# Kernel optimization log

Hardware: AMD Instinct MI355X
Metric: run time of the kernel (lower is better)

## Reference

```python
import jax, jax.numpy as jnp
import numpy as np

K = 3  # number of propagation hops in SGConv


def setup_inputs() -> dict:
    key = jax.random.key(0)
    k1, k2, k3, k4 = jax.random.split(key, 4)
    N, E, F_in, F_out = 100000, 1600000, 32, 64
    x = jax.random.normal(k1, (N, F_in), dtype=jnp.float32)
    edge_index = jax.random.randint(k2, (2, E), 0, N, dtype=jnp.int64)
    # Linear(in_channels, hidden_channels) params, torch layout: W [out, in], b [out]
    lim = 1.0 / np.sqrt(F_in)
    W = jax.random.uniform(k3, (F_out, F_in), minval=-lim, maxval=lim, dtype=jnp.float32)
    b = jax.random.uniform(k4, (F_out,), minval=-lim, maxval=lim, dtype=jnp.float32)
    return {"x": x, "edge_index": edge_index, "W": W, "b": b}


def reference(x, edge_index, W, b):
    N = x.shape[0]
    # gcn_norm: add self-loops with weight 1, symmetric normalization
    loop = jnp.arange(N, dtype=edge_index.dtype)
    src = jnp.concatenate([edge_index[0], loop])  # [E+N] message sources (x_j)
    dst = jnp.concatenate([edge_index[1], loop])  # [E+N] aggregation targets
    ones = jnp.ones(src.shape[0], dtype=x.dtype)
    deg = jax.ops.segment_sum(ones, dst, num_segments=N)  # in-degree incl. self-loop
    dinv = jnp.where(deg > 0, jax.lax.rsqrt(deg), 0.0)
    norm = dinv[src] * dinv[dst]  # [E+N]
    # K hops of normalized sparse propagation: x <- \hat{A} x
    h = x
    for _ in range(K):
        h = jax.ops.segment_sum(norm[:, None] * h[src], dst, num_segments=N)
    # final linear transform
    return h @ W.T + b
```

## Files before the change

kernel.cpp:

```cpp
#include <hip/hip_runtime.h>


#define F_IN 32
#define F_OUT 64
#define SB_SHIFT 13
#define NSB_MAX 16
#define SUB_SHIFT 8
#define SUB (1 << SUB_SHIFT)
#define SPS 32
#define EPB1 2048
#define EPB2 4096
#define SCAP 147456
#define SUBCAP 6144
#define BPS (SCAP / EPB2)

typedef float f4 __attribute__((ext_vector_type(4)));
typedef float f8 __attribute__((ext_vector_type(8)));
typedef _Float16 h4 __attribute__((ext_vector_type(4)));
typedef _Float16 h8 __attribute__((ext_vector_type(8)));
typedef int i2 __attribute__((ext_vector_type(2)));

__global__ __launch_bounds__(256) void k_bin1(const int* __restrict__ ei,
                                              int* __restrict__ scur,
                                              unsigned* __restrict__ b1, int E) {
    __shared__ unsigned stage[EPB1];
    __shared__ unsigned char bidl[EPB1];
    __shared__ int h4w[4][NSB_MAX];
    __shared__ int f4w[4][NSB_MAX];
    __shared__ int lscanx[NSB_MAX], lbase[NSB_MAX];
    unsigned rec[EPB1 / 256];
    int      bk[EPB1 / 256];
    int tid = threadIdx.x;
    int wv = tid >> 6;
    int base = blockIdx.x * EPB1;
    int cnt = E - base; if (cnt > EPB1) cnt = EPB1;

    if (tid < 64) { h4w[tid >> 4][tid & 15] = 0; }
    __syncthreads();
#pragma unroll
    for (int k = 0; k < EPB1 / 256; ++k) {
        int i = base + k * 256 + tid;
        bk[k] = -1;
        if (i < E) {
            unsigned s = (unsigned)ei[i];
            unsigned d = (unsigned)ei[E + i];
            int b = d >> SB_SHIFT;
            rec[k] = (s << SB_SHIFT) | (d & ((1u << SB_SHIFT) - 1));
            bk[k] = b;
            atomicAdd(&h4w[wv][b], 1);
        }
    }
    __syncthreads();
    if (tid < 16) {
        int t0 = h4w[0][tid], t1 = h4w[1][tid], t2 = h4w[2][tid], t3 = h4w[3][tid];
        int tot = t0 + t1 + t2 + t3;
        int inc = tot;
#pragma unroll
        for (int off = 1; off < 16; off <<= 1) {
            int t = __shfl_up(inc, off);
            if (tid >= off) inc += t;
        }
        int excl = inc - tot;
        lscanx[tid] = excl;
        lbase[tid] = tot ? atomicAdd(&scur[tid], tot) : 0;
        f4w[0][tid] = excl;
        f4w[1][tid] = excl + t0;
        f4w[2][tid] = excl + t0 + t1;
        f4w[3][tid] = excl + t0 + t1 + t2;
    }
    __syncthreads();
#pragma unroll
    for (int k = 0; k < EPB1 / 256; ++k) {
        if (bk[k] >= 0) {
            int loc = atomicAdd(&f4w[wv][bk[k]], 1);
            stage[loc] = rec[k];
            bidl[loc] = (unsigned char)bk[k];
        }
    }
    __syncthreads();
    for (int k = 0; k < EPB1 / 256; ++k) {
        int idx = k * 256 + tid;
        if (idx < cnt) {
            int b = bidl[idx];
            b1[(size_t)b * SCAP + lbase[b] + (idx - lscanx[b])] = stage[idx];
        }
    }
}

__global__ __launch_bounds__(256) void k_bin2(const unsigned* __restrict__ b1,
                                              const int* __restrict__ scur,
                                              int* __restrict__ subcur,
                                              unsigned* __restrict__ b2) {
    int sb = blockIdx.x / BPS;
    int base = (blockIdx.x % BPS) * EPB2;
    int count = scur[sb];
    if (base >= count) return;
    int cnt = count - base; if (cnt > EPB2) cnt = EPB2;
    const unsigned* src = b1 + (size_t)sb * SCAP + base;

    __shared__ unsigned stage[EPB2];
    __shared__ unsigned char bidl[EPB2];
    __shared__ int h4w[4][SPS];
    __shared__ int f4w[4][SPS];
    __shared__ int lscanx[SPS], lbase[SPS];
    unsigned rec[EPB2 / 256];
    int tid = threadIdx.x;
    int wv = tid >> 6;
    if (tid < 128) h4w[tid >> 5][tid & 31] = 0;
    __syncthreads();
#pragma unroll
    for (int k = 0; k < EPB2 / 256; ++k) {
        int i = k * 256 + tid;
        rec[k] = 0xFFFFFFFFu;
        if (i < cnt) {
            unsigned r = src[i];
            rec[k] = r;
            atomicAdd(&h4w[wv][(r >> SUB_SHIFT) & (SPS - 1)], 1);
        }
    }
    __syncthreads();
    if (tid < 32) {
        int t0 = h4w[0][tid], t1 = h4w[1][tid], t2 = h4w[2][tid], t3 = h4w[3][tid];
        int tot = t0 + t1 + t2 + t3;
        int inc = tot;
#pragma unroll
        for (int off = 1; off < 32; off <<= 1) {
            int t = __shfl_up(inc, off);
            if (tid >= off) inc += t;
        }
        int excl = inc - tot;
        lscanx[tid] = excl;
        lbase[tid] = tot ? atomicAdd(&subcur[sb * SPS + tid], tot) : 0;
        f4w[0][tid] = excl;
        f4w[1][tid] = excl + t0;
        f4w[2][tid] = excl + t0 + t1;
        f4w[3][tid] = excl + t0 + t1 + t2;
    }
    __syncthreads();
#pragma unroll
    for (int k = 0; k < EPB2 / 256; ++k) {
        if (rec[k] != 0xFFFFFFFFu) {
            int b = (rec[k] >> SUB_SHIFT) & (SPS - 1);
            int loc = atomicAdd(&f4w[wv][b], 1);
            stage[loc] = rec[k];
            bidl[loc] = (unsigned char)b;
        }
    }
    __syncthreads();
    for (int k = 0; k < EPB2 / 256; ++k) {
        int idx = k * 256 + tid;
        if (idx < cnt) {
            unsigned r = stage[idx];
            int b = bidl[idx];
            unsigned packed = ((r >> SB_SHIFT) << SUB_SHIFT) | (r & (SUB - 1));
            b2[(size_t)(sb * SPS + b) * SUBCAP + lbase[b] + (idx - lscanx[b])] = packed;
        }
    }
}

__global__ __launch_bounds__(256) void k_fill3(const unsigned* __restrict__ b2,
                                               const int* __restrict__ subcur,
                                               const f4* __restrict__ x,
                                               float* __restrict__ dinv,
                                               i2* __restrict__ rp2,
                                               int* __restrict__ col,
                                               h8* __restrict__ g0, int N) {
    __shared__ unsigned stage[SUBCAP];
    __shared__ int h[SUB];
    __shared__ float dl[SUB];
    __shared__ int wsum[4];
    int tid = threadIdx.x;
    int g = blockIdx.x;
    int count = subcur[g];
    int sbase = g * SUBCAP;
    int n0 = g << SUB_SHIFT;

    h[tid] = 0;
    for (int e = tid; e < count; e += 256) stage[e] = b2[(size_t)sbase + e];
    __syncthreads();
    for (int e = tid; e < count; e += 256) atomicAdd(&h[stage[e] & (SUB - 1)], 1);
    __syncthreads();

    int deg = h[tid];
    int lane = tid & 63, wid = tid >> 6;
    int inc = deg;
#pragma unroll
    for (int off = 1; off < 64; off <<= 1) {
        int t = __shfl_up(inc, off);
        if (lane >= off) inc += t;
    }
    if (lane == 63) wsum[wid] = inc;
    __syncthreads();
    if (wid == 0) {
        int v = (lane < 4) ? wsum[lane] : 0;
#pragma unroll
        for (int off = 1; off < 4; off <<= 1) {
            int t = __shfl_up(v, off);
            if (lane >= off) v += t;
        }
        if (lane < 4) wsum[lane] = v;
    }
    __syncthreads();
    int incl = inc + (wid ? wsum[wid - 1] : 0);
    int excl = incl - deg;

    int node = n0 + tid;
    float di = rsqrtf(1.0f + (float)deg);
    dl[tid] = di;
    if (node < N) {
        dinv[node] = di;
        rp2[node] = (i2){sbase + excl, sbase + incl};
    }
    h[tid] = excl;
    __syncthreads();

    for (int e = tid; e < count; e += 256) {
        unsigned r = stage[e];
        int slot = sbase + atomicAdd(&h[r & (SUB - 1)], 1);
        col[slot] = (int)(r >> SUB_SHIFT);
    }

    for (int idx = tid; idx < SUB * 4; idx += 256) {
        int nl = idx >> 2;
        int q = idx & 3;
        int node2 = n0 + nl;
        if (node2 < N) {
            int gi = node2 * 8 + q * 2;
            f4 vlo = dl[nl] * x[gi];
            f4 vhi = dl[nl] * x[gi + 1];
            f8 v = __builtin_shufflevector(vlo, vhi, 0, 1, 2, 3, 4, 5, 6, 7);
            g0[(size_t)node2 * 4 + q] = __builtin_convertvector(v, h8);
        }
    }
}

__global__ __launch_bounds__(256) void k_hop_gather(const i2* __restrict__ rp2,
                                                    const int* __restrict__ col,
                                                    const float* __restrict__ dinv,
                                                    const h8* __restrict__ gin,
                                                    h8* __restrict__ gout, int N) {
    int t = blockIdx.x * blockDim.x + threadIdx.x;
    int n = t >> 2;
    if (n >= N) return;
    int q = t & 3;
    i2 r2 = rp2[n];
    int e0 = r2.x, e1 = r2.y;
    f8 a0 = __builtin_convertvector(gin[(size_t)n * 4 + q], f8);
    f8 a1 = {0.f, 0.f, 0.f, 0.f, 0.f, 0.f, 0.f, 0.f};
    int e = e0;
    for (; e + 3 < e1; e += 4) {
        int s0 = col[e], s1 = col[e + 1], s2 = col[e + 2], s3 = col[e + 3];
        h8 h0 = gin[(size_t)s0 * 4 + q];
        h8 h1 = gin[(size_t)s1 * 4 + q];
        h8 h2 = gin[(size_t)s2 * 4 + q];
        h8 h3 = gin[(size_t)s3 * 4 + q];
        a0 += __builtin_convertvector(h0, f8);
        a1 += __builtin_convertvector(h1, f8);
        a0 += __builtin_convertvector(h2, f8);
        a1 += __builtin_convertvector(h3, f8);
    }
    for (; e < e1; ++e) a0 += __builtin_convertvector(gin[(size_t)col[e] * 4 + q], f8);
    float di = dinv[n];
    float sc = di * di;
    f8 r = sc * (a0 + a1);
    gout[(size_t)n * 4 + q] = __builtin_convertvector(r, h8);
}

__global__ __launch_bounds__(256) void k_hop3_linear(const i2* __restrict__ rp2,
                                                     const int* __restrict__ col,
                                                     const float* __restrict__ dinv,
                                                     const h8* __restrict__ gin,
                                                     const float* __restrict__ W,
                                                     const float* __restrict__ bias,
                                                     float* __restrict__ out, int N) {
    __shared__ float Wl[F_OUT][F_IN + 1];
    __shared__ float hl[64][F_IN + 1];
    int tid = threadIdx.x;
    for (int idx = tid; idx < F_OUT * F_IN; idx += 256)
        Wl[idx >> 5][idx & 31] = W[idx];

    int nl = tid >> 2;
    int q = tid & 3;
    int nbase = blockIdx.x * 64;
    int n = nbase + nl;
    if (n < N) {
        i2 r2 = rp2[n];
        int e0 = r2.x, e1 = r2.y;
        f8 a0 = __builtin_convertvector(gin[(size_t)n * 4 + q], f8);
        f8 a1 = {0.f, 0.f, 0.f, 0.f, 0.f, 0.f, 0.f, 0.f};
        int e = e0;
        for (; e + 3 < e1; e += 4) {
            int s0 = col[e], s1 = col[e + 1], s2 = col[e + 2], s3 = col[e + 3];
            h8 h0 = gin[(size_t)s0 * 4 + q];
            h8 h1 = gin[(size_t)s1 * 4 + q];
            h8 h2 = gin[(size_t)s2 * 4 + q];
            h8 h3 = gin[(size_t)s3 * 4 + q];
            a0 += __builtin_convertvector(h0, f8);
            a1 += __builtin_convertvector(h1, f8);
            a0 += __builtin_convertvector(h2, f8);
            a1 += __builtin_convertvector(h3, f8);
        }
        for (; e < e1; ++e) a0 += __builtin_convertvector(gin[(size_t)col[e] * 4 + q], f8);
        float di = dinv[n];
        f8 r = di * (a0 + a1);
#pragma unroll
        for (int i = 0; i < 8; ++i) hl[nl][q * 8 + i] = r[i];
    }
    __syncthreads();
    int o = tid & 63;
    float wreg[F_IN];
#pragma unroll
    for (int f = 0; f < F_IN; ++f) wreg[f] = Wl[o][f];
    float bv = bias[o];
    int nchunk = tid >> 6;
#pragma unroll
    for (int p = 0; p < 16; ++p) {
        int nloc = p * 4 + nchunk;
        int nn = nbase + nloc;
        if (nn < N) {
            float acc = bv;
#pragma unroll
            for (int f = 0; f < F_IN; ++f) acc += hl[nloc][f] * wreg[f];
            out[(size_t)nn * F_OUT + o] = acc;
        }
    }
}

extern "C" void kernel_launch(void* const* d_in, const int* in_sizes, int n_in,
                              void* d_out, int out_size, void* d_ws, size_t ws_size,
                              hipStream_t stream) {
    const float* x  = (const float*)d_in[0];
    const int*   ei = (const int*)d_in[1];
    const float* W  = (const float*)d_in[2];
    const float* b  = (const float*)d_in[3];
    float* out = (float*)d_out;

    const int N = in_sizes[0] / F_IN;
    const int E = in_sizes[1] / 2;
    const int NSB  = (N + (1 << SB_SHIFT) - 1) >> SB_SHIFT;
    const int NSUB = (N + SUB - 1) >> SUB_SHIFT;

    int* scur   = (int*)d_ws;
    int* subcur = scur + NSB_MAX;
    i2*  rp2    = (i2*)(subcur + NSB_MAX * SPS);
    float* dinv = (float*)(rp2 + N);
    unsigned* b1 = (unsigned*)(((uintptr_t)(dinv + N) + 255) & ~(uintptr_t)255);
    unsigned* b2 = b1 + (size_t)NSB_MAX * SCAP;
    int* col     = (int*)(b2 + (size_t)NSB_MAX * SPS * SUBCAP);
    _Float16* hA = (_Float16*)(((uintptr_t)(col + (size_t)NSB_MAX * SPS * SUBCAP) + 255)
                               & ~(uintptr_t)255);
    _Float16* hB  = hA + (size_t)N * F_IN;
    _Float16* hB2 = hB + (size_t)N * F_IN;

    const int B = 256;
    dim3 blk(B);

    hipMemsetAsync(scur, 0, (NSB_MAX + NSB_MAX * SPS) * sizeof(int), stream);

    k_bin1<<<dim3((E + EPB1 - 1) / EPB1), blk, 0, stream>>>(ei, scur, b1, E);
    k_bin2<<<dim3(NSB * BPS), blk, 0, stream>>>(b1, scur, subcur, b2);

    k_fill3<<<dim3(NSUB), blk, 0, stream>>>(b2, subcur, (const f4*)x,
                                            dinv, rp2, col, (h8*)hA, N);

    dim3 gHop(((size_t)N * 4 + B - 1) / B);
    k_hop_gather<<<gHop, blk, 0, stream>>>(rp2, col, dinv, (const h8*)hA, (h8*)hB, N);
    k_hop_gather<<<gHop, blk, 0, stream>>>(rp2, col, dinv, (const h8*)hB, (h8*)hB2, N);

    k_hop3_linear<<<dim3((N + 63) / 64), blk, 0, stream>>>(rp2, col, dinv,
                                                           (const h8*)hB2, W, b, out, N);
}
```

Measured before the change: 200.3 us.

## Split feature halves into separate arrays and pack per-node CSR records

Features are split into two 16-feature half arrays, each 3.2 MB in fp16. Each hop kernel now processes one half at a time, with block IDs interleaved so that concurrently running blocks touch the same half, which is meant to make gather reads hit in cache. Row pointers and dinv are packed into one int4 record per node, and each row is padded to a multiple of 4 so column indices can be read as int4 loads. The third hop is no longer fused with the linear layer, so a separate k_linear kernel and one extra launch plus a write and read of the intermediate are added.

Result: slower. 225.8 us (+12.7%).

```diff
diff --git a/kernel.cpp b/kernel.cpp
--- a/kernel.cpp
+++ b/kernel.cpp
@@ -16,7 +16,6 @@
 
 typedef float f4 __attribute__((ext_vector_type(4)));
 typedef float f8 __attribute__((ext_vector_type(8)));
-typedef _Float16 h4 __attribute__((ext_vector_type(4)));
 typedef _Float16 h8 __attribute__((ext_vector_type(8)));
 typedef int i2 __attribute__((ext_vector_type(2)));
 
@@ -161,10 +160,10 @@
 __global__ __launch_bounds__(256) void k_fill3(const unsigned* __restrict__ b2,
                                                const int* __restrict__ subcur,
                                                const f4* __restrict__ x,
-                                               float* __restrict__ dinv,
-                                               i2* __restrict__ rp2,
+                                               int4* __restrict__ nrec,
                                                int* __restrict__ col,
-                                               h8* __restrict__ g0, int N) {
+                                               h8* __restrict__ g_lo,
+                                               h8* __restrict__ g_hi, int N) {
     __shared__ unsigned stage[SUBCAP];
     __shared__ int h[SUB];
     __shared__ float dl[SUB];
@@ -182,8 +181,9 @@
     __syncthreads();
 
     int deg = h[tid];
+    int pdeg = (deg + 3) & ~3;
     int lane = tid & 63, wid = tid >> 6;
-    int inc = deg;
+    int inc = pdeg;
 #pragma unroll
     for (int off = 1; off < 64; off <<= 1) {
         int t = __shfl_up(inc, off);
@@ -202,16 +202,16 @@
     }
     __syncthreads();
     int incl = inc + (wid ? wsum[wid - 1] : 0);
-    int excl = incl - deg;
+    int exclp = incl - pdeg;
 
     int node = n0 + tid;
     float di = rsqrtf(1.0f + (float)deg);
     dl[tid] = di;
     if (node < N) {
-        dinv[node] = di;
-        rp2[node] = (i2){sbase + excl, sbase + incl};
-    }
-    h[tid] = excl;
+        int e0a = sbase + exclp;
+        nrec[node] = make_int4(e0a, e0a + deg, __float_as_int(di), 0);
+    }
+    h[tid] = exclp;
     __syncthreads();
 
     for (int e = tid; e < count; e += 256) {
@@ -229,82 +229,75 @@
             f4 vlo = dl[nl] * x[gi];
             f4 vhi = dl[nl] * x[gi + 1];
             f8 v = __builtin_shufflevector(vlo, vhi, 0, 1, 2, 3, 4, 5, 6, 7);
-            g0[(size_t)node2 * 4 + q] = __builtin_convertvector(v, h8);
-        }
-    }
-}
-
-__global__ __launch_bounds__(256) void k_hop_gather(const i2* __restrict__ rp2,
-                                                    const int* __restrict__ col,
-                                                    const float* __restrict__ dinv,
-                                                    const h8* __restrict__ gin,
-                                                    h8* __restrict__ gout, int N) {
-    int t = blockIdx.x * blockDim.x + threadIdx.x;
-    int n = t >> 2;
+            h8 hv = __builtin_convertvector(v, h8);
+            if (q < 2) g_lo[(size_t)node2 * 2 + q] = hv;
+            else       g_hi[(size_t)node2 * 2 + (q - 2)] = hv;
+        }
+    }
+}
+
+__global__ __launch_bounds__(256) void k_hop_half(const int4* __restrict__ nrec,
+                                                  const int* __restrict__ col,
+                                                  const h8* __restrict__ gin_lo,
+                                                  const h8* __restrict__ gin_hi,
+                                                  h8* __restrict__ gout_lo,
+                                                  h8* __restrict__ gout_hi,
+                                                  int N, int hblocks, int isfinal) {
+    int bid = blockIdx.x;
+    int grp = bid & 7;
+    int lblk = (bid >> 3) * 4 + (grp & 3);
+    if (lblk >= hblocks) return;
+    const h8* __restrict__ gin  = (grp < 4) ? gin_lo  : gin_hi;
+    h8*       __restrict__ gout = (grp < 4) ? gout_lo : gout_hi;
+    int t = lblk * 256 + threadIdx.x;
+    int n = t >> 1;
     if (n >= N) return;
-    int q = t & 3;
-    i2 r2 = rp2[n];
-    int e0 = r2.x, e1 = r2.y;
-    f8 a0 = __builtin_convertvector(gin[(size_t)n * 4 + q], f8);
+    int q = t & 1;
+    int4 r = nrec[n];
+    int e0 = r.x, e1 = r.y;
+    float di = __int_as_float(r.z);
+    f8 a0 = __builtin_convertvector(gin[(size_t)n * 2 + q], f8);
     f8 a1 = {0.f, 0.f, 0.f, 0.f, 0.f, 0.f, 0.f, 0.f};
     int e = e0;
     for (; e + 3 < e1; e += 4) {
-        int s0 = col[e], s1 = col[e + 1], s2 = col[e + 2], s3 = col[e + 3];
-        h8 h0 = gin[(size_t)s0 * 4 + q];
-        h8 h1 = gin[(size_t)s1 * 4 + q];
-        h8 h2 = gin[(size_t)s2 * 4 + q];
-        h8 h3 = gin[(size_t)s3 * 4 + q];
+        int4 c4 = *(const int4*)(col + e);
+        h8 h0 = gin[(size_t)c4.x * 2 + q];
+        h8 h1 = gin[(size_t)c4.y * 2 + q];
+        h8 h2 = gin[(size_t)c4.z * 2 + q];
+        h8 h3 = gin[(size_t)c4.w * 2 + q];
         a0 += __builtin_convertvector(h0, f8);
         a1 += __builtin_convertvector(h1, f8);
         a0 += __builtin_convertvector(h2, f8);
         a1 += __builtin_convertvector(h3, f8);
     }
-    for (; e < e1; ++e) a0 += __builtin_convertvector(gin[(size_t)col[e] * 4 + q], f8);
-    float di = dinv[n];
-    float sc = di * di;
-    f8 r = sc * (a0 + a1);
-    gout[(size_t)n * 4 + q] = __builtin_convertvector(r, h8);
-}
-
-__global__ __launch_bounds__(256) void k_hop3_linear(const i2* __restrict__ rp2,
-                                                     const int* __restrict__ col,
-                                                     const float* __restrict__ dinv,
-                                                     const h8* __restrict__ gin,
-                                                     const float* __restrict__ W,
-                                                     const float* __restrict__ bias,
-                                                     float* __restrict__ out, int N) {
+    for (; e < e1; ++e) a0 += __builtin_convertvector(gin[(size_t)col[e] * 2 + q], f8);
+    float sc = isfinal ? di : di * di;
+    f8 rr = sc * (a0 + a1);
+    gout[(size_t)n * 2 + q] = __builtin_convertvector(rr, h8);
+}
+
+__global__ __launch_bounds__(256) void k_linear(const h8* __restrict__ lo,
+                                                const h8* __restrict__ hi,
+                                                const float* __restrict__ W,
+                                                const float* __restrict__ bias,
+                                                float* __restrict__ out, int N) {
     __shared__ float Wl[F_OUT][F_IN + 1];
     __shared__ float hl[64][F_IN + 1];
     int tid = threadIdx.x;
     for (int idx = tid; idx < F_OUT * F_IN; idx += 256)
         Wl[idx >> 5][idx & 31] = W[idx];
 
-    int nl = tid >> 2;
-    int q = tid & 3;
     int nbase = blockIdx.x * 64;
-    int n = nbase + nl;
-    if (n < N) {
-        i2 r2 = rp2[n];
-        int e0 = r2.x, e1 = r2.y;
-        f8 a0 = __builtin_convertvector(gin[(size_t)n * 4 + q], f8);
-        f8 a1 = {0.f, 0.f, 0.f, 0.f, 0.f, 0.f, 0.f, 0.f};
-        int e = e0;
-        for (; e + 3 < e1; e += 4) {
-            int s0 = col[e], s1 = col[e + 1], s2 = col[e + 2], s3 = col[e + 3];
-            h8 h0 = gin[(size_t)s0 * 4 + q];
-            h8 h1 = gin[(size_t)s1 * 4 + q];
-            h8 h2 = gin[(size_t)s2 * 4 + q];
-            h8 h3 = gin[(size_t)s3 * 4 + q];
-            a0 += __builtin_convertvector(h0, f8);
-            a1 += __builtin_convertvector(h1, f8);
-            a0 += __builtin_convertvector(h2, f8);
-            a1 += __builtin_convertvector(h3, f8);
-        }
-        for (; e < e1; ++e) a0 += __builtin_convertvector(gin[(size_t)col[e] * 4 + q], f8);
-        float di = dinv[n];
-        f8 r = di * (a0 + a1);
-#pragma unroll
-        for (int i = 0; i < 8; ++i) hl[nl][q * 8 + i] = r[i];
+    {
+        int nl = tid >> 2;
+        int c = tid & 3;
+        int n = nbase + nl;
+        if (n < N) {
+            h8 v = (c < 2) ? lo[(size_t)n * 2 + c] : hi[(size_t)n * 2 + (c - 2)];
+            f8 f = __builtin_convertvector(v, f8);
+#pragma unroll
+            for (int i = 0; i < 8; ++i) hl[nl][c * 8 + i] = f[i];
+        }
     }
     __syncthreads();
     int o = tid & 63;
@@ -342,15 +335,17 @@
 
     int* scur   = (int*)d_ws;
     int* subcur = scur + NSB_MAX;
-    i2*  rp2    = (i2*)(subcur + NSB_MAX * SPS);
-    float* dinv = (float*)(rp2 + N);
-    unsigned* b1 = (unsigned*)(((uintptr_t)(dinv + N) + 255) & ~(uintptr_t)255);
+    int4* nrec  = (int4*)(((uintptr_t)(subcur + NSB_MAX * SPS) + 255) & ~(uintptr_t)255);
+    unsigned* b1 = (unsigned*)(((uintptr_t)(nrec + N) + 255) & ~(uintptr_t)255);
     unsigned* b2 = b1 + (size_t)NSB_MAX * SCAP;
     int* col     = (int*)(b2 + (size_t)NSB_MAX * SPS * SUBCAP);
-    _Float16* hA = (_Float16*)(((uintptr_t)(col + (size_t)NSB_MAX * SPS * SUBCAP) + 255)
-                               & ~(uintptr_t)255);
-    _Float16* hB  = hA + (size_t)N * F_IN;
-    _Float16* hB2 = hB + (size_t)N * F_IN;
+    _Float16* hbase = (_Float16*)(((uintptr_t)(col + (size_t)NSB_MAX * SPS * SUBCAP) + 255)
+                                  & ~(uintptr_t)255);
+    const size_t HALF = (size_t)N * (F_IN / 2);
+    _Float16* hAlo = hbase;
+    _Float16* hAhi = hAlo + HALF;
+    _Float16* hBlo = hAhi + HALF;
+    _Float16* hBhi = hBlo + HALF;
 
     const int B = 256;
     dim3 blk(B);
@@ -361,12 +356,17 @@
     k_bin2<<<dim3(NSB * BPS), blk, 0, stream>>>(b1, scur, subcur, b2);
 
     k_fill3<<<dim3(NSUB), blk, 0, stream>>>(b2, subcur, (const f4*)x,
-                                            dinv, rp2, col, (h8*)hA, N);
-
-    dim3 gHop(((size_t)N * 4 + B - 1) / B);
-    k_hop_gather<<<gHop, blk, 0, stream>>>(rp2, col, dinv, (const h8*)hA, (h8*)hB, N);
-    k_hop_gather<<<gHop, blk, 0, stream>>>(rp2, col, dinv, (const h8*)hB, (h8*)hB2, N);
-
-    k_hop3_linear<<<dim3((N + 63) / 64), blk, 0, stream>>>(rp2, col, dinv,
-                                                           (const h8*)hB2, W, b, out, N);
-}
+                                            nrec, col, (h8*)hAlo, (h8*)hAhi, N);
+
+    const int HB = (N * 2 + B - 1) / B;
+    dim3 gHop(8 * ((HB + 3) / 4));
+    k_hop_half<<<gHop, blk, 0, stream>>>(nrec, col, (const h8*)hAlo, (const h8*)hAhi,
+                                         (h8*)hBlo, (h8*)hBhi, N, HB, 0);
+    k_hop_half<<<gHop, blk, 0, stream>>>(nrec, col, (const h8*)hBlo, (const h8*)hBhi,
+                                         (h8*)hAlo, (h8*)hAhi, N, HB, 0);
+    k_hop_half<<<gHop, blk, 0, stream>>>(nrec, col, (const h8*)hAlo, (const h8*)hAhi,
+                                         (h8*)hBlo, (h8*)hBhi, N, HB, 1);
+
+    k_linear<<<dim3((N + 63) / 64), blk, 0, stream>>>((const h8*)hBlo, (const h8*)hBhi,
+                                                      W, b, out, N);
+}
```

## Pack node records, pad CSR rows for vector col loads, add nontemporal hints

Applied to the files above, without the earlier changes.

Merges the row-pointer pair and dinv into a single 16-byte per-node record, so one load replaces two. Each node's edge segment is padded to a multiple of four, which lets column indices be fetched as aligned int4 loads with a software-prefetched next group. Nontemporal loads and stores are applied to streaming data (x, col, records, outputs), and the hop buffers are ping-ponged to drop one feature buffer. This cuts load instructions and cache pollution in the gather kernels, at the cost of padding slack in each subgroup's col capacity.

New measurement: 206.7 us. +3.2%, slower.

```diff
diff --git a/kernel.cpp b/kernel.cpp
--- a/kernel.cpp
+++ b/kernel.cpp
@@ -16,9 +16,8 @@
 
 typedef float f4 __attribute__((ext_vector_type(4)));
 typedef float f8 __attribute__((ext_vector_type(8)));
-typedef _Float16 h4 __attribute__((ext_vector_type(4)));
 typedef _Float16 h8 __attribute__((ext_vector_type(8)));
-typedef int i2 __attribute__((ext_vector_type(2)));
+typedef int i4 __attribute__((ext_vector_type(4)));
 
 __global__ __launch_bounds__(256) void k_bin1(const int* __restrict__ ei,
                                               int* __restrict__ scur,
@@ -161,8 +160,7 @@
 __global__ __launch_bounds__(256) void k_fill3(const unsigned* __restrict__ b2,
                                                const int* __restrict__ subcur,
                                                const f4* __restrict__ x,
-                                               float* __restrict__ dinv,
-                                               i2* __restrict__ rp2,
+                                               i4* __restrict__ nrec,
                                                int* __restrict__ col,
                                                h8* __restrict__ g0, int N) {
     __shared__ unsigned stage[SUBCAP];
@@ -182,8 +180,9 @@
     __syncthreads();
 
     int deg = h[tid];
+    int pdeg = (deg + 3) & ~3;
     int lane = tid & 63, wid = tid >> 6;
-    int inc = deg;
+    int inc = pdeg;
 #pragma unroll
     for (int off = 1; off < 64; off <<= 1) {
         int t = __shfl_up(inc, off);
@@ -202,16 +201,16 @@
     }
     __syncthreads();
     int incl = inc + (wid ? wsum[wid - 1] : 0);
-    int excl = incl - deg;
+    int exclp = incl - pdeg;
 
     int node = n0 + tid;
     float di = rsqrtf(1.0f + (float)deg);
     dl[tid] = di;
     if (node < N) {
-        dinv[node] = di;
-        rp2[node] = (i2){sbase + excl, sbase + incl};
-    }
-    h[tid] = excl;
+        int e0a = sbase + exclp;
+        nrec[node] = (i4){e0a, e0a + deg, (int)__float_as_int(di), 0};
+    }
+    h[tid] = exclp;
     __syncthreads();
 
     for (int e = tid; e < count; e += 256) {
@@ -226,49 +225,58 @@
         int node2 = n0 + nl;
         if (node2 < N) {
             int gi = node2 * 8 + q * 2;
-            f4 vlo = dl[nl] * x[gi];
-            f4 vhi = dl[nl] * x[gi + 1];
+            f4 vlo = dl[nl] * __builtin_nontemporal_load(&x[gi]);
+            f4 vhi = dl[nl] * __builtin_nontemporal_load(&x[gi + 1]);
             f8 v = __builtin_shufflevector(vlo, vhi, 0, 1, 2, 3, 4, 5, 6, 7);
-            g0[(size_t)node2 * 4 + q] = __builtin_convertvector(v, h8);
-        }
-    }
-}
-
-__global__ __launch_bounds__(256) void k_hop_gather(const i2* __restrict__ rp2,
+            __builtin_nontemporal_store(__builtin_convertvector(v, h8),
+                                        &g0[(size_t)node2 * 4 + q]);
+        }
+    }
+}
+
+__global__ __launch_bounds__(256) void k_hop_gather(const i4* __restrict__ nrec,
                                                     const int* __restrict__ col,
-                                                    const float* __restrict__ dinv,
                                                     const h8* __restrict__ gin,
                                                     h8* __restrict__ gout, int N) {
     int t = blockIdx.x * blockDim.x + threadIdx.x;
     int n = t >> 2;
     if (n >= N) return;
     int q = t & 3;
-    i2 r2 = rp2[n];
-    int e0 = r2.x, e1 = r2.y;
+    i4 r = __builtin_nontemporal_load(&nrec[n]);
+    int e0 = r.x, e1 = r.y;
+    float di = __int_as_float(r.z);
     f8 a0 = __builtin_convertvector(gin[(size_t)n * 4 + q], f8);
     f8 a1 = {0.f, 0.f, 0.f, 0.f, 0.f, 0.f, 0.f, 0.f};
     int e = e0;
-    for (; e + 3 < e1; e += 4) {
-        int s0 = col[e], s1 = col[e + 1], s2 = col[e + 2], s3 = col[e + 3];
-        h8 h0 = gin[(size_t)s0 * 4 + q];
-        h8 h1 = gin[(size_t)s1 * 4 + q];
-        h8 h2 = gin[(size_t)s2 * 4 + q];
-        h8 h3 = gin[(size_t)s3 * 4 + q];
-        a0 += __builtin_convertvector(h0, f8);
-        a1 += __builtin_convertvector(h1, f8);
-        a0 += __builtin_convertvector(h2, f8);
-        a1 += __builtin_convertvector(h3, f8);
+    if (e + 3 < e1) {
+        i4 c4 = __builtin_nontemporal_load((const i4*)(col + e));
+        for (;;) {
+            int en = e + 4;
+            bool more = (en + 3 < e1);
+            i4 cn;
+            if (more) cn = __builtin_nontemporal_load((const i4*)(col + en));
+            h8 h0 = gin[(size_t)c4.x * 4 + q];
+            h8 h1 = gin[(size_t)c4.y * 4 + q];
+            h8 h2 = gin[(size_t)c4.z * 4 + q];
+            h8 h3 = gin[(size_t)c4.w * 4 + q];
+            a0 += __builtin_convertvector(h0, f8);
+            a1 += __builtin_convertvector(h1, f8);
+            a0 += __builtin_convertvector(h2, f8);
+            a1 += __builtin_convertvector(h3, f8);
+            e = en;
+            if (!more) break;
+            c4 = cn;
+        }
     }
     for (; e < e1; ++e) a0 += __builtin_convertvector(gin[(size_t)col[e] * 4 + q], f8);
-    float di = dinv[n];
     float sc = di * di;
-    f8 r = sc * (a0 + a1);
-    gout[(size_t)n * 4 + q] = __builtin_convertvector(r, h8);
-}
-
-__global__ __launch_bounds__(256) void k_hop3_linear(const i2* __restrict__ rp2,
+    f8 rr = sc * (a0 + a1);
+    __builtin_nontemporal_store(__builtin_convertvector(rr, h8),
+                                &gout[(size_t)n * 4 + q]);
+}
+
+__global__ __launch_bounds__(256) void k_hop3_linear(const i4* __restrict__ nrec,
                                                      const int* __restrict__ col,
-                                                     const float* __restrict__ dinv,
                                                      const h8* __restrict__ gin,
                                                      const float* __restrict__ W,
                                                      const float* __restrict__ bias,
@@ -284,27 +292,37 @@
     int nbase = blockIdx.x * 64;
     int n = nbase + nl;
     if (n < N) {
-        i2 r2 = rp2[n];
-        int e0 = r2.x, e1 = r2.y;
+        i4 r = __builtin_nontemporal_load(&nrec[n]);
+        int e0 = r.x, e1 = r.y;
+        float di = __int_as_float(r.z);
         f8 a0 = __builtin_convertvector(gin[(size_t)n * 4 + q], f8);
         f8 a1 = {0.f, 0.f, 0.f, 0.f, 0.f, 0.f, 0.f, 0.f};
         int e = e0;
-        for (; e + 3 < e1; e += 4) {
-            int s0 = col[e], s1 = col[e + 1], s2 = col[e + 2], s3 = col[e + 3];
-            h8 h0 = gin[(size_t)s0 * 4 + q];
-            h8 h1 = gin[(size_t)s1 * 4 + q];
-            h8 h2 = gin[(size_t)s2 * 4 + q];
-            h8 h3 = gin[(size_t)s3 * 4 + q];
-            a0 += __builtin_convertvector(h0, f8);
-            a1 += __builtin_convertvector(h1, f8);
-            a0 += __builtin_convertvector(h2, f8);
-            a1 += __builtin_convertvector(h3, f8);
+        if (e + 3 < e1) {
+            i4 c4 = __builtin_nontemporal_load((const i4*)(col + e));
+            for (;;) {
+                int en = e + 4;
+                bool more = (en + 3 < e1);
+                i4 cn;
+                if (more) cn = __builtin_nontemporal_load((const i4*)(col + en));
+                h8 h0 = gin[(size_t)c4.x * 4 + q];
+                h8 h1 = gin[(size_t)c4.y * 4 + q];
+                h8 h2 = gin[(size_t)c4.z * 4 + q];
+                h8 h3 = gin[(size_t)c4.w * 4 + q];
+                a0 += __builtin_convertvector(h0, f8);
+                a1 += __builtin_convertvector(h1, f8);
+                a0 += __builtin_convertvector(h2, f8);
+                a1 += __builtin_convertvector(h3, f8);
+                e = en;
+                if (!more) break;
+                c4 = cn;
+            }
         }
         for (; e < e1; ++e) a0 += __builtin_convertvector(gin[(size_t)col[e] * 4 + q], f8);
-        float di = dinv[n];
-        f8 r = di * (a0 + a1);
-#pragma unroll
-        for (int i = 0; i < 8; ++i) hl[nl][q * 8 + i] = r[i];
+        float di2 = di;
+        f8 rr = di2 * (a0 + a1);
+#pragma unroll
+        for (int i = 0; i < 8; ++i) hl[nl][q * 8 + i] = rr[i];
     }
     __syncthreads();
     int o = tid & 63;
@@ -321,7 +339,7 @@
             float acc = bv;
 #pragma unroll
             for (int f = 0; f < F_IN; ++f) acc += hl[nloc][f] * wreg[f];
-            out[(size_t)nn * F_OUT + o] = acc;
+            __builtin_nontemporal_store(acc, &out[(size_t)nn * F_OUT + o]);
         }
     }
 }
@@ -342,15 +360,13 @@
 
     int* scur   = (int*)d_ws;
     int* subcur = scur + NSB_MAX;
-    i2*  rp2    = (i2*)(subcur + NSB_MAX * SPS);
-    float* dinv = (float*)(rp2 + N);
-    unsigned* b1 = (unsigned*)(((uintptr_t)(dinv + N) + 255) & ~(uintptr_t)255);
+    i4* nrec    = (i4*)(((uintptr_t)(subcur + NSB_MAX * SPS) + 255) & ~(uintptr_t)255);
+    unsigned* b1 = (unsigned*)(((uintptr_t)(nrec + N) + 255) & ~(uintptr_t)255);
     unsigned* b2 = b1 + (size_t)NSB_MAX * SCAP;
     int* col     = (int*)(b2 + (size_t)NSB_MAX * SPS * SUBCAP);
     _Float16* hA = (_Float16*)(((uintptr_t)(col + (size_t)NSB_MAX * SPS * SUBCAP) + 255)
                                & ~(uintptr_t)255);
-    _Float16* hB  = hA + (size_t)N * F_IN;
-    _Float16* hB2 = hB + (size_t)N * F_IN;
+    _Float16* hB = hA + (size_t)N * F_IN;
 
     const int B = 256;
     dim3 blk(B);
@@ -361,12 +377,12 @@
     k_bin2<<<dim3(NSB * BPS), blk, 0, stream>>>(b1, scur, subcur, b2);
 
     k_fill3<<<dim3(NSUB), blk, 0, stream>>>(b2, subcur, (const f4*)x,
-                                            dinv, rp2, col, (h8*)hA, N);
+                                            nrec, col, (h8*)hA, N);
 
     dim3 gHop(((size_t)N * 4 + B - 1) / B);
-    k_hop_gather<<<gHop, blk, 0, stream>>>(rp2, col, dinv, (const h8*)hA, (h8*)hB, N);
-    k_hop_gather<<<gHop, blk, 0, stream>>>(rp2, col, dinv, (const h8*)hB, (h8*)hB2, N);
-
-    k_hop3_linear<<<dim3((N + 63) / 64), blk, 0, stream>>>(rp2, col, dinv,
-                                                           (const h8*)hB2, W, b, out, N);
-}
+    k_hop_gather<<<gHop, blk, 0, stream>>>(nrec, col, (const h8*)hA, (h8*)hB, N);
+    k_hop_gather<<<gHop, blk, 0, stream>>>(nrec, col, (const h8*)hB, (h8*)hA, N);
+
+    k_hop3_linear<<<dim3((N + 63) / 64), blk, 0, stream>>>(nrec, col,
+                                                           (const h8*)hA, W, b, out, N);
+}
```

## Split neighbor lists by source half and barrier-sync gathers for L2 locality

Applied to the files above, without the earlier changes.

The CSR build now orders each node's neighbors so sources in the lower half of the node range come first, and records that split point in a packed per-node record together with the row range and dinv. The gather kernels handle the low-half neighbors, hit a block barrier, then handle the high half, so that blocks tend to touch the same half of the feature table at the same time and get more cache reuse. Index loads and output stores use nontemporal hints, and the hop buffers ping-pong between two arrays instead of three. The cost is extra shared-memory atomics in the fill kernel and a barrier inside the gather loop, which can stall warps that have uneven degrees.

New measurement: 212.6 us. 1.06x slower.

```diff
diff --git a/kernel.cpp b/kernel.cpp
--- a/kernel.cpp
+++ b/kernel.cpp
@@ -16,9 +16,8 @@
 
 typedef float f4 __attribute__((ext_vector_type(4)));
 typedef float f8 __attribute__((ext_vector_type(8)));
-typedef _Float16 h4 __attribute__((ext_vector_type(4)));
 typedef _Float16 h8 __attribute__((ext_vector_type(8)));
-typedef int i2 __attribute__((ext_vector_type(2)));
+typedef int i4 __attribute__((ext_vector_type(4)));
 
 __global__ __launch_bounds__(256) void k_bin1(const int* __restrict__ ei,
                                               int* __restrict__ scur,
@@ -161,12 +160,12 @@
 __global__ __launch_bounds__(256) void k_fill3(const unsigned* __restrict__ b2,
                                                const int* __restrict__ subcur,
                                                const f4* __restrict__ x,
-                                               float* __restrict__ dinv,
-                                               i2* __restrict__ rp2,
+                                               i4* __restrict__ nrec,
                                                int* __restrict__ col,
-                                               h8* __restrict__ g0, int N) {
+                                               h8* __restrict__ g0, int N, int Nhalf) {
     __shared__ unsigned stage[SUBCAP];
     __shared__ int h[SUB];
+    __shared__ int hlo[SUB];
     __shared__ float dl[SUB];
     __shared__ int wsum[4];
     int tid = threadIdx.x;
@@ -176,12 +175,19 @@
     int n0 = g << SUB_SHIFT;
 
     h[tid] = 0;
+    hlo[tid] = 0;
     for (int e = tid; e < count; e += 256) stage[e] = b2[(size_t)sbase + e];
     __syncthreads();
-    for (int e = tid; e < count; e += 256) atomicAdd(&h[stage[e] & (SUB - 1)], 1);
+    for (int e = tid; e < count; e += 256) {
+        unsigned r = stage[e];
+        int nd = r & (SUB - 1);
+        atomicAdd(&h[nd], 1);
+        if ((int)(r >> SUB_SHIFT) < Nhalf) atomicAdd(&hlo[nd], 1);
+    }
     __syncthreads();
 
     int deg = h[tid];
+    int dlo = hlo[tid];
     int lane = tid & 63, wid = tid >> 6;
     int inc = deg;
 #pragma unroll
@@ -208,16 +214,19 @@
     float di = rsqrtf(1.0f + (float)deg);
     dl[tid] = di;
     if (node < N) {
-        dinv[node] = di;
-        rp2[node] = (i2){sbase + excl, sbase + incl};
+        int e0a = sbase + excl;
+        nrec[node] = (i4){e0a, e0a + deg, (int)__float_as_int(di), e0a + dlo};
     }
     h[tid] = excl;
+    hlo[tid] = excl + dlo;
     __syncthreads();
 
     for (int e = tid; e < count; e += 256) {
         unsigned r = stage[e];
-        int slot = sbase + atomicAdd(&h[r & (SUB - 1)], 1);
-        col[slot] = (int)(r >> SUB_SHIFT);
+        int nd = r & (SUB - 1);
+        int src = (int)(r >> SUB_SHIFT);
+        int slot = (src < Nhalf) ? atomicAdd(&h[nd], 1) : atomicAdd(&hlo[nd], 1);
+        col[sbase + slot] = src;
     }
 
     for (int idx = tid; idx < SUB * 4; idx += 256) {
@@ -234,22 +243,30 @@
     }
 }
 
-__global__ __launch_bounds__(256) void k_hop_gather(const i2* __restrict__ rp2,
+__global__ __launch_bounds__(256) void k_hop_gather(const i4* __restrict__ nrec,
                                                     const int* __restrict__ col,
-                                                    const float* __restrict__ dinv,
                                                     const h8* __restrict__ gin,
                                                     h8* __restrict__ gout, int N) {
     int t = blockIdx.x * blockDim.x + threadIdx.x;
     int n = t >> 2;
-    if (n >= N) return;
     int q = t & 3;
-    i2 r2 = rp2[n];
-    int e0 = r2.x, e1 = r2.y;
-    f8 a0 = __builtin_convertvector(gin[(size_t)n * 4 + q], f8);
+    bool act = n < N;
+    int e0 = 0, e1 = 0, es = 0;
+    float di = 0.f;
+    f8 a0 = {0.f, 0.f, 0.f, 0.f, 0.f, 0.f, 0.f, 0.f};
     f8 a1 = {0.f, 0.f, 0.f, 0.f, 0.f, 0.f, 0.f, 0.f};
+    if (act) {
+        i4 r = __builtin_nontemporal_load(&nrec[n]);
+        e0 = r.x; e1 = r.y; es = r.w;
+        di = __int_as_float(r.z);
+        a0 = __builtin_convertvector(gin[(size_t)n * 4 + q], f8);
+    }
     int e = e0;
-    for (; e + 3 < e1; e += 4) {
-        int s0 = col[e], s1 = col[e + 1], s2 = col[e + 2], s3 = col[e + 3];
+    for (; e + 3 < es; e += 4) {
+        int s0 = __builtin_nontemporal_load(col + e);
+        int s1 = __builtin_nontemporal_load(col + e + 1);
+        int s2 = __builtin_nontemporal_load(col + e + 2);
+        int s3 = __builtin_nontemporal_load(col + e + 3);
         h8 h0 = gin[(size_t)s0 * 4 + q];
         h8 h1 = gin[(size_t)s1 * 4 + q];
         h8 h2 = gin[(size_t)s2 * 4 + q];
@@ -259,16 +276,35 @@
         a0 += __builtin_convertvector(h2, f8);
         a1 += __builtin_convertvector(h3, f8);
     }
-    for (; e < e1; ++e) a0 += __builtin_convertvector(gin[(size_t)col[e] * 4 + q], f8);
-    float di = dinv[n];
-    float sc = di * di;
-    f8 r = sc * (a0 + a1);
-    gout[(size_t)n * 4 + q] = __builtin_convertvector(r, h8);
-}
-
-__global__ __launch_bounds__(256) void k_hop3_linear(const i2* __restrict__ rp2,
+    for (; e < es; ++e)
+        a0 += __builtin_convertvector(gin[(size_t)__builtin_nontemporal_load(col + e) * 4 + q], f8);
+    __syncthreads();
+    for (; e + 3 < e1; e += 4) {
+        int s0 = __builtin_nontemporal_load(col + e);
+        int s1 = __builtin_nontemporal_load(col + e + 1);
+        int s2 = __builtin_nontemporal_load(col + e + 2);
+        int s3 = __builtin_nontemporal_load(col + e + 3);
+        h8 h0 = gin[(size_t)s0 * 4 + q];
+        h8 h1 = gin[(size_t)s1 * 4 + q];
+        h8 h2 = gin[(size_t)s2 * 4 + q];
+        h8 h3 = gin[(size_t)s3 * 4 + q];
+        a0 += __builtin_convertvector(h0, f8);
+        a1 += __builtin_convertvector(h1, f8);
+        a0 += __builtin_convertvector(h2, f8);
+        a1 += __builtin_convertvector(h3, f8);
+    }
+    for (; e < e1; ++e)
+        a0 += __builtin_convertvector(gin[(size_t)__builtin_nontemporal_load(col + e) * 4 + q], f8);
+    if (act) {
+        float sc = di * di;
+        f8 rr = sc * (a0 + a1);
+        __builtin_nontemporal_store(__builtin_convertvector(rr, h8),
+                                    &gout[(size_t)n * 4 + q]);
+    }
+}
+
+__global__ __launch_bounds__(256) void k_hop3_linear(const i4* __restrict__ nrec,
                                                      const int* __restrict__ col,
-                                                     const float* __restrict__ dinv,
                                                      const h8* __restrict__ gin,
                                                      const float* __restrict__ W,
                                                      const float* __restrict__ bias,
@@ -283,28 +319,55 @@
     int q = tid & 3;
     int nbase = blockIdx.x * 64;
     int n = nbase + nl;
-    if (n < N) {
-        i2 r2 = rp2[n];
-        int e0 = r2.x, e1 = r2.y;
-        f8 a0 = __builtin_convertvector(gin[(size_t)n * 4 + q], f8);
-        f8 a1 = {0.f, 0.f, 0.f, 0.f, 0.f, 0.f, 0.f, 0.f};
-        int e = e0;
-        for (; e + 3 < e1; e += 4) {
-            int s0 = col[e], s1 = col[e + 1], s2 = col[e + 2], s3 = col[e + 3];
-            h8 h0 = gin[(size_t)s0 * 4 + q];
-            h8 h1 = gin[(size_t)s1 * 4 + q];
-            h8 h2 = gin[(size_t)s2 * 4 + q];
-            h8 h3 = gin[(size_t)s3 * 4 + q];
-            a0 += __builtin_convertvector(h0, f8);
-            a1 += __builtin_convertvector(h1, f8);
-            a0 += __builtin_convertvector(h2, f8);
-            a1 += __builtin_convertvector(h3, f8);
-        }
-        for (; e < e1; ++e) a0 += __builtin_convertvector(gin[(size_t)col[e] * 4 + q], f8);
-        float di = dinv[n];
-        f8 r = di * (a0 + a1);
-#pragma unroll
-        for (int i = 0; i < 8; ++i) hl[nl][q * 8 + i] = r[i];
+    bool act = n < N;
+    int e0 = 0, e1 = 0, es = 0;
+    float di = 0.f;
+    f8 a0 = {0.f, 0.f, 0.f, 0.f, 0.f, 0.f, 0.f, 0.f};
+    f8 a1 = {0.f, 0.f, 0.f, 0.f, 0.f, 0.f, 0.f, 0.f};
+    if (act) {
+        i4 r = __builtin_nontemporal_load(&nrec[n]);
+        e0 = r.x; e1 = r.y; es = r.w;
+        di = __int_as_float(r.z);
+        a0 = __builtin_convertvector(gin[(size_t)n * 4 + q], f8);
+    }
+    int e = e0;
+    for (; e + 3 < es; e += 4) {
+        int s0 = __builtin_nontemporal_load(col + e);
+        int s1 = __builtin_nontemporal_load(col + e + 1);
+        int s2 = __builtin_nontemporal_load(col + e + 2);
+        int s3 = __builtin_nontemporal_load(col + e + 3);
+        h8 h0 = gin[(size_t)s0 * 4 + q];
+        h8 h1 = gin[(size_t)s1 * 4 + q];
+        h8 h2 = gin[(size_t)s2 * 4 + q];
+        h8 h3 = gin[(size_t)s3 * 4 + q];
+        a0 += __builtin_convertvector(h0, f8);
+        a1 += __builtin_convertvector(h1, f8);
+        a0 += __builtin_convertvector(h2, f8);
+        a1 += __builtin_convertvector(h3, f8);
+    }
+    for (; e < es; ++e)
+        a0 += __builtin_convertvector(gin[(size_t)__builtin_nontemporal_load(col + e) * 4 + q], f8);
+    __syncthreads();
+    for (; e + 3 < e1; e += 4) {
+        int s0 = __builtin_nontemporal_load(col + e);
+        int s1 = __builtin_nontemporal_load(col + e + 1);
+        int s2 = __builtin_nontemporal_load(col + e + 2);
+        int s3 = __builtin_nontemporal_load(col + e + 3);
+        h8 h0 = gin[(size_t)s0 * 4 + q];
+        h8 h1 = gin[(size_t)s1 * 4 + q];
+        h8 h2 = gin[(size_t)s2 * 4 + q];
+        h8 h3 = gin[(size_t)s3 * 4 + q];
+        a0 += __builtin_convertvector(h0, f8);
+        a1 += __builtin_convertvector(h1, f8);
+        a0 += __builtin_convertvector(h2, f8);
+        a1 += __builtin_convertvector(h3, f8);
+    }
+    for (; e < e1; ++e)
+        a0 += __builtin_convertvector(gin[(size_t)__builtin_nontemporal_load(col + e) * 4 + q], f8);
+    if (act) {
+        f8 rr = di * (a0 + a1);
+#pragma unroll
+        for (int i = 0; i < 8; ++i) hl[nl][q * 8 + i] = rr[i];
     }
     __syncthreads();
     int o = tid & 63;
@@ -339,18 +402,17 @@
     const int E = in_sizes[1] / 2;
     const int NSB  = (N + (1 << SB_SHIFT) - 1) >> SB_SHIFT;
     const int NSUB = (N + SUB - 1) >> SUB_SHIFT;
+    const int Nhalf = N >> 1;
 
     int* scur   = (int*)d_ws;
     int* subcur = scur + NSB_MAX;
-    i2*  rp2    = (i2*)(subcur + NSB_MAX * SPS);
-    float* dinv = (float*)(rp2 + N);
-    unsigned* b1 = (unsigned*)(((uintptr_t)(dinv + N) + 255) & ~(uintptr_t)255);
+    i4* nrec    = (i4*)(((uintptr_t)(subcur + NSB_MAX * SPS) + 255) & ~(uintptr_t)255);
+    unsigned* b1 = (unsigned*)(((uintptr_t)(nrec + N) + 255) & ~(uintptr_t)255);
     unsigned* b2 = b1 + (size_t)NSB_MAX * SCAP;
     int* col     = (int*)(b2 + (size_t)NSB_MAX * SPS * SUBCAP);
     _Float16* hA = (_Float16*)(((uintptr_t)(col + (size_t)NSB_MAX * SPS * SUBCAP) + 255)
                                & ~(uintptr_t)255);
-    _Float16* hB  = hA + (size_t)N * F_IN;
-    _Float16* hB2 = hB + (size_t)N * F_IN;
+    _Float16* hB = hA + (size_t)N * F_IN;
 
     const int B = 256;
     dim3 blk(B);
@@ -361,12 +423,12 @@
     k_bin2<<<dim3(NSB * BPS), blk, 0, stream>>>(b1, scur, subcur, b2);
 
     k_fill3<<<dim3(NSUB), blk, 0, stream>>>(b2, subcur, (const f4*)x,
-                                            dinv, rp2, col, (h8*)hA, N);
+                                            nrec, col, (h8*)hA, N, Nhalf);
 
     dim3 gHop(((size_t)N * 4 + B - 1) / B);
-    k_hop_gather<<<gHop, blk, 0, stream>>>(rp2, col, dinv, (const h8*)hA, (h8*)hB, N);
-    k_hop_gather<<<gHop, blk, 0, stream>>>(rp2, col, dinv, (const h8*)hB, (h8*)hB2, N);
-
-    k_hop3_linear<<<dim3((N + 63) / 64), blk, 0, stream>>>(rp2, col, dinv,
-                                                           (const h8*)hB2, W, b, out, N);
-}
+    k_hop_gather<<<gHop, blk, 0, stream>>>(nrec, col, (const h8*)hA, (h8*)hB, N);
+    k_hop_gather<<<gHop, blk, 0, stream>>>(nrec, col, (const h8*)hB, (h8*)hA, N);
+
+    k_hop3_linear<<<dim3((N + 63) / 64), blk, 0, stream>>>(nrec, col,
+                                                           (const h8*)hA, W, b, out, N);
+}
```
